# Optimization experiments

Hardware: AMD Instinct MI355X
Metric: run time of the kernel (lower is better)

The kernel has to match this reference:

```python
import jax, jax.numpy as jnp
import numpy as np

N_HEAD = 12
NEG_INF = -1e30


def setup_inputs() -> dict:
    key = jax.random.key(0)
    ks = jax.random.split(key, 12)
    bs, q_len, c_len, d = 2, 2048, 2048, 768
    s = 1.0 / np.sqrt(d)
    return {
        "query": jax.random.normal(ks[0], (bs, q_len, d), jnp.float32),
        "context": jax.random.normal(ks[1], (bs, c_len, d), jnp.float32),
        "c_mask": jax.random.randint(ks[2], (bs, c_len), 0, 2, jnp.int32),
        "Wq_w": jax.random.normal(ks[3], (d, d), jnp.float32) * s,
        "Wq_b": jnp.zeros((d,), jnp.float32),
        "Wk_w": jax.random.normal(ks[4], (d, d), jnp.float32) * s,
        "Wk_b": jnp.zeros((d,), jnp.float32),
        "Wv_w": jax.random.normal(ks[5], (d, d), jnp.float32) * s,
        "Wv_b": jnp.zeros((d,), jnp.float32),
        "fc_w": jax.random.normal(ks[6], (d, d), jnp.float32) * s,
        "fc_b": jnp.zeros((d,), jnp.float32),
    }


def reference(query, context, c_mask, Wq_w, Wq_b, Wk_w, Wk_b, Wv_w, Wv_b, fc_w, fc_b):
    bs, q_len, d = query.shape
    c_len = context.shape[1]
    d_k = d // N_HEAD
    a = 1.0 / np.sqrt(d_k)

    # QKV projections (torch Linear: y = x @ W.T + b), split into heads
    q = (query @ Wq_w.T + Wq_b).reshape(bs, q_len, N_HEAD, d_k)
    k = (context @ Wk_w.T + Wk_b).reshape(bs, c_len, N_HEAD, d_k)
    v = (context @ Wv_w.T + Wv_b).reshape(bs, c_len, N_HEAD, d_k)

    # scores [bs, n_head, q_len, c_len]
    s = jnp.einsum('bqhd,bchd->bhqc', q, k) * a

    # mask_logits: s * m + (1 - m) * -1e30, mask broadcast over heads and q
    m = c_mask.astype(s.dtype)[:, None, None, :]
    s = s * m + (1.0 - m) * NEG_INF

    p = jax.nn.softmax(s, axis=-1)  # dropout p=0.0 -> identity

    out = jnp.einsum('bhqc,bchd->bqhd', p, v).reshape(bs, q_len, d)
    return out @ fc_w.T + fc_b
```

## Files before the change

### kernel.cpp

```cpp
#include <hip/hip_runtime.h>
#include <cstdint>

#define D_MODEL 768
#define NH      12
#define DKH     64
#define SEQ     2048
#define BS      2
#define MROWS   (BS*SEQ)

typedef __bf16 bf16x8 __attribute__((ext_vector_type(8)));
typedef float  f32x4  __attribute__((ext_vector_type(4)));
typedef unsigned int u32_as1 __attribute__((address_space(1)));
typedef unsigned int u32_as3 __attribute__((address_space(3)));

__device__ __forceinline__ void gld16(const void* g, void* l) {
  __builtin_amdgcn_global_load_lds((const u32_as1*)g, (u32_as3*)l, 16, 0, 0);
}
__device__ __forceinline__ unsigned short f2bf(float x) {
  return __builtin_bit_cast(unsigned short, (__bf16)x);
}

__global__ void cvt2(const float* __restrict__ a, const float* __restrict__ b,
                     unsigned short* __restrict__ oa, unsigned short* __restrict__ ob) {
  const float* in = blockIdx.y ? b : a;
  unsigned short* out = blockIdx.y ? ob : oa;
  int i = blockIdx.x * 256 + threadIdx.x;
  float4 v = reinterpret_cast<const float4*>(in)[i];
  ushort4 o; o.x = f2bf(v.x); o.y = f2bf(v.y); o.z = f2bf(v.z); o.w = f2bf(v.w);
  reinterpret_cast<ushort4*>(out)[i] = o;
}
__global__ void cvt4(const float* __restrict__ a, const float* __restrict__ b,
                     const float* __restrict__ c, const float* __restrict__ d,
                     unsigned short* __restrict__ oa, unsigned short* __restrict__ ob,
                     unsigned short* __restrict__ oc, unsigned short* __restrict__ od) {
  const float* in; unsigned short* out;
  switch (blockIdx.y) {
    case 0: in = a; out = oa; break;
    case 1: in = b; out = ob; break;
    case 2: in = c; out = oc; break;
    default: in = d; out = od; break;
  }
  int i = blockIdx.x * 256 + threadIdx.x;
  float4 v = reinterpret_cast<const float4*>(in)[i];
  ushort4 o; o.x = f2bf(v.x); o.y = f2bf(v.y); o.z = f2bf(v.z); o.w = f2bf(v.w);
  reinterpret_cast<ushort4*>(out)[i] = o;
}

__global__ void mask_bf(const int* __restrict__ m, unsigned short* __restrict__ o) {
  int i = blockIdx.x * 256 + threadIdx.x;
  o[i] = f2bf(m[i] ? 1.0f : 0.0f);
}

template<bool OUT_F32>
__device__ __forceinline__ void gemm64x128_body(
    const unsigned short* __restrict__ A, const unsigned short* __restrict__ B,
    const float* __restrict__ bias, int biasRow, void* __restrict__ Cout,
    int ldc, int m0, int n0, float outScale, const int* __restrict__ colMask)
{
  __shared__ alignas(16) char sA[2][8192];
  __shared__ alignas(16) char sB[2][16384];
  const int tid = threadIdx.x;
  const int w = tid >> 6, l = tid & 63;
  const int g16 = l >> 4, c16 = l & 15;
  const int wr = (w >> 1) * 32, wc = (w & 1) * 64;

  auto stageA = [&](int kt, char* dst) {
#pragma unroll
    for (int i = 0; i < 2; i++) {
      int ch = w * 2 + i;
      int X = ch * 1024 + l * 16;
      int row = X >> 7;
      int sl = ((X >> 4) & 7) ^ (row & 7);
      gld16(A + (size_t)(m0 + row) * 768 + kt + sl * 8, dst + ch * 1024);
    }
  };
  auto stageB = [&](int kt, char* dst) {
#pragma unroll
    for (int i = 0; i < 4; i++) {
      int ch = w * 4 + i;
      int X = ch * 1024 + l * 16;
      int row = X >> 7;
      int sl = ((X >> 4) & 7) ^ (row & 7);
      gld16(B + (size_t)(n0 + row) * 768 + kt + sl * 8, dst + ch * 1024);
    }
  };

  f32x4 acc[2][4];
#pragma unroll
  for (int m = 0; m < 2; m++)
#pragma unroll
    for (int n = 0; n < 4; n++) acc[m][n] = f32x4{0.f, 0.f, 0.f, 0.f};

  stageA(0, sA[0]);
  stageB(0, sB[0]);
  __syncthreads();
  int cur = 0;
  for (int kt = 0; kt < 768; kt += 64) {
    if (kt + 64 < 768) {
      stageA(kt + 64, sA[cur ^ 1]);
      stageB(kt + 64, sB[cur ^ 1]);
    }
    __builtin_amdgcn_s_setprio(1);
#pragma unroll
    for (int kk = 0; kk < 2; kk++) {
      bf16x8 af[2], bq[4];
#pragma unroll
      for (int m = 0; m < 2; m++) {
        int row = wr + m * 16 + c16, slot = kk * 4 + g16;
        af[m] = *(const bf16x8*)(sA[cur] + row * 128 + ((slot ^ (row & 7)) << 4));
      }
#pragma unroll
      for (int n = 0; n < 4; n++) {
        int row = wc + n * 16 + c16, slot = kk * 4 + g16;
        bq[n] = *(const bf16x8*)(sB[cur] + row * 128 + ((slot ^ (row & 7)) << 4));
      }
#pragma unroll
      for (int m = 0; m < 2; m++)
#pragma unroll
        for (int n = 0; n < 4; n++)
          acc[m][n] = __builtin_amdgcn_mfma_f32_16x16x32_bf16(af[m], bq[n], acc[m][n], 0, 0, 0);
    }
    __builtin_amdgcn_s_setprio(0);
    __syncthreads();
    cur ^= 1;
  }

#pragma unroll
  for (int m = 0; m < 2; m++)
#pragma unroll
    for (int n = 0; n < 4; n++)
#pragma unroll
      for (int r = 0; r < 4; r++) {
        int row = m0 + wr + m * 16 + g16 * 4 + r;
        int col = n0 + wc + n * 16 + c16;
        float v = (acc[m][n][r] + (biasRow ? bias[row] : bias[col])) * outScale;
        if (colMask) v *= (float)colMask[col];
        if constexpr (OUT_F32) ((float*)Cout)[(size_t)row * ldc + col] = v;
        else ((unsigned short*)Cout)[(size_t)row * ldc + col] = f2bf(v);
      }
}

#define QSCALE 0.1803368801111f

__global__ __launch_bounds__(256, 2) void gemm_qkv(
    const unsigned short* __restrict__ q_bf, const unsigned short* __restrict__ c_bf,
    const unsigned short* __restrict__ wq, const unsigned short* __restrict__ wk,
    const unsigned short* __restrict__ wv,
    const float* __restrict__ bq, const float* __restrict__ bk,
    const float* __restrict__ bv, const int* __restrict__ cmask,
    unsigned short* __restrict__ Qb, unsigned short* __restrict__ Kb,
    unsigned short* __restrict__ Vtb)
{
  const int x = blockIdx.x;
  const int lin = (x & 7) * 48 + (x >> 3);
  if (blockIdx.y == 0) {
    gemm64x128_body<false>(q_bf, wq, bq, 0, Qb, 768, (lin / 6) * 64, (lin % 6) * 128,
                           QSCALE, nullptr);
  } else if (blockIdx.y == 1) {
    gemm64x128_body<false>(c_bf, wk, bk, 0, Kb, 768, (lin / 6) * 64, (lin % 6) * 128,
                           1.0f, nullptr);
  } else {
    gemm64x128_body<false>(wv, c_bf, bv, 1, Vtb, 4096, (lin % 12) * 64, (lin / 12) * 128,
                           1.0f, cmask);
  }
}

__global__ __launch_bounds__(256, 2) void gemm_fc(
    const unsigned short* __restrict__ Ob, const unsigned short* __restrict__ wf,
    const float* __restrict__ fb, float* __restrict__ out)
{
  const int x = blockIdx.x;
  const int lin = (x & 7) * 48 + (x >> 3);
  gemm64x128_body<true>(Ob, wf, fb, 0, out, 768, (lin / 6) * 64, (lin % 6) * 128,
                        1.0f, nullptr);
}

__global__ __launch_bounds__(256, 4) void attn_kernel(
    const unsigned short* __restrict__ Qb, const unsigned short* __restrict__ Kb,
    const unsigned short* __restrict__ Vt, const unsigned short* __restrict__ maskbf,
    unsigned short* __restrict__ Ob)
{
  __shared__ alignas(16) char sK[2][8192];
  __shared__ alignas(16) char sV[2][8192];
  __shared__ alignas(16) char sP[8192];
  const int tid = threadIdx.x, w = tid >> 6, l = tid & 63;
  const int g16 = l >> 4, c16 = l & 15;
  const int flat = blockIdx.x;
  const int xcd = flat & 7, sidx = flat >> 3;
  const int p = xcd + 8 * (sidx >> 5);
  const int qt = sidx & 31;
  const int h = p % 12, b = p / 12;
  const int qrow0 = b * SEQ + qt * 64;
  const int crow0 = b * SEQ;

  bf16x8 qa[2];
  {
    const unsigned short* qp =
        Qb + (size_t)(qrow0 + w * 16 + c16) * D_MODEL + h * DKH + g16 * 8;
    qa[0] = *(const bf16x8*)(qp);
    qa[1] = *(const bf16x8*)(qp + 32);
  }

  auto stageK = [&](int ct, int buf) {
#pragma unroll
    for (int i = 0; i < 2; i++) {
      int ch = w * 2 + i;
      int X = ch * 1024 + l * 16;
      int row = X >> 7;
      int sl = ((X >> 4) & 7) ^ (row & 7);
      gld16(Kb + (size_t)(crow0 + ct + row) * D_MODEL + h * DKH + sl * 8,
            sK[buf] + ch * 1024);
    }
  };
  auto stageV = [&](int ct, int buf) {
#pragma unroll
    for (int i = 0; i < 2; i++) {
      int ch = w * 2 + i;
      int X = ch * 1024 + l * 16;
      int row = X >> 7;
      int sl = ((X >> 4) & 7) ^ (row & 7);
      gld16(Vt + (size_t)(h * DKH + row) * (size_t)MROWS + crow0 + ct + sl * 8,
            sV[buf] + ch * 1024);
    }
  };

  f32x4 accO[4], accL;
#pragma unroll
  for (int n = 0; n < 4; n++) accO[n] = f32x4{0.f, 0.f, 0.f, 0.f};
  accL = f32x4{0.f, 0.f, 0.f, 0.f};

  stageK(0, 0); stageV(0, 0);
  __syncthreads();
  int cur = 0;

  for (int ct = 0; ct < SEQ; ct += 64) {
    if (ct + 64 < SEQ) { stageK(ct + 64, cur ^ 1); stageV(ct + 64, cur ^ 1); }

    bf16x8 mfrag[2];
#pragma unroll
    for (int kk = 0; kk < 2; kk++)
      mfrag[kk] = *(const bf16x8*)(maskbf + crow0 + ct + kk * 32 + g16 * 8);

    f32x4 s[4];
#pragma unroll
    for (int n = 0; n < 4; n++) s[n] = f32x4{0.f, 0.f, 0.f, 0.f};
    __builtin_amdgcn_s_setprio(1);
#pragma unroll
    for (int kk = 0; kk < 2; kk++) {
      bf16x8 kf[4];
#pragma unroll
      for (int n = 0; n < 4; n++) {
        int row = n * 16 + c16, slot = kk * 4 + g16;
        kf[n] = *(const bf16x8*)(sK[cur] + row * 128 + ((slot ^ (row & 7)) << 4));
      }
#pragma unroll
      for (int n = 0; n < 4; n++)
        s[n] = __builtin_amdgcn_mfma_f32_16x16x32_bf16(qa[kk], kf[n], s[n], 0, 0, 0);
    }
    __builtin_amdgcn_s_setprio(0);

#pragma unroll
    for (int r = 0; r < 4; r++) {
      int prow = g16 * 4 + r;
#pragma unroll
      for (int n = 0; n < 4; n++) {
        float pv = __builtin_amdgcn_exp2f(s[n][r]);
        int slot = n * 2 + (c16 >> 3);
        int addr = w * 2048 + prow * 128 + ((slot ^ (prow & 7)) << 4) + (c16 & 7) * 2;
        *(__bf16*)(sP + addr) = (__bf16)pv;
      }
    }

    __builtin_amdgcn_s_setprio(1);
#pragma unroll
    for (int kk = 0; kk < 2; kk++) {
      bf16x8 pa, vf[4];
      {
        int prow = c16, slot = kk * 4 + g16;
        pa = *(const bf16x8*)(sP + w * 2048 + prow * 128 + ((slot ^ (prow & 7)) << 4));
      }
#pragma unroll
      for (int n = 0; n < 4; n++) {
        int vrow = n * 16 + c16, slot = kk * 4 + g16;
        vf[n] = *(const bf16x8*)(sV[cur] + vrow * 128 + ((slot ^ (vrow & 7)) << 4));
      }
#pragma unroll
      for (int n = 0; n < 4; n++)
        accO[n] = __builtin_amdgcn_mfma_f32_16x16x32_bf16(pa, vf[n], accO[n], 0, 0, 0);
      accL = __builtin_amdgcn_mfma_f32_16x16x32_bf16(pa, mfrag[kk], accL, 0, 0, 0);
    }
    __builtin_amdgcn_s_setprio(0);

    __syncthreads();
    cur ^= 1;
  }

#pragma unroll
  for (int r = 0; r < 4; r++) {
    float inv = 1.0f / accL[r];
#pragma unroll
    for (int n = 0; n < 4; n++) {
      int row = qrow0 + w * 16 + g16 * 4 + r;
      int col = h * DKH + n * 16 + c16;
      Ob[(size_t)row * D_MODEL + col] = f2bf(accO[n][r] * inv);
    }
  }
}

extern "C" void kernel_launch(void* const* d_in, const int* in_sizes, int n_in,
                              void* d_out, int out_size, void* d_ws, size_t ws_size,
                              hipStream_t stream) {
  const float* query   = (const float*)d_in[0];
  const float* context = (const float*)d_in[1];
  const int*   cmask   = (const int*)d_in[2];
  const float* Wq_w = (const float*)d_in[3];
  const float* Wq_b = (const float*)d_in[4];
  const float* Wk_w = (const float*)d_in[5];
  const float* Wk_b = (const float*)d_in[6];
  const float* Wv_w = (const float*)d_in[7];
  const float* Wv_b = (const float*)d_in[8];
  const float* fc_w = (const float*)d_in[9];
  const float* fc_b = (const float*)d_in[10];
  float* out = (float*)d_out;

  unsigned short* ws   = (unsigned short*)d_ws;
  const size_t NQ = (size_t)MROWS * D_MODEL;
  const size_t NW = (size_t)D_MODEL * D_MODEL;
  unsigned short* q_bf = ws;
  unsigned short* c_bf = q_bf + NQ;
  unsigned short* Qb   = c_bf + NQ;
  unsigned short* Kb   = Qb + NQ;
  unsigned short* Vtb  = Kb + NQ;
  unsigned short* Ob   = Vtb + NQ;
  unsigned short* wq   = Ob + NQ;
  unsigned short* wk   = wq + NW;
  unsigned short* wv   = wk + NW;
  unsigned short* wf   = wv + NW;
  unsigned short* maskbf = q_bf;

  cvt2<<<dim3(NQ / 4 / 256, 2), 256, 0, stream>>>(query, context, q_bf, c_bf);
  cvt4<<<dim3(NW / 4 / 256, 4), 256, 0, stream>>>(Wq_w, Wk_w, Wv_w, fc_w, wq, wk, wv, wf);

  gemm_qkv<<<dim3(384, 3), 256, 0, stream>>>(
      q_bf, c_bf, wq, wk, wv, Wq_b, Wk_b, Wv_b, cmask, Qb, Kb, Vtb);

  mask_bf<<<MROWS / 256, 256, 0, stream>>>(cmask, maskbf);

  attn_kernel<<<768, 256, 0, stream>>>(Qb, Kb, Vtb, maskbf, Ob);

  gemm_fc<<<384, 256, 0, stream>>>(Ob, wf, fc_b, out);
}
```

Measured before the change: 100.3 us.

## Double attention query tile to 128 rows per block for K/V reuse

Each attention block now processes 128 query rows instead of 64, with every wave handling two 16-row sub-tiles that share the K and V fragments loaded from shared memory. This halves the number of blocks and the total K/V staging traffic from global memory per unit of work, and amortizes LDS reads of K/V across two MFMA rows. In exchange, register and LDS use per block roughly doubles, launch bounds drop to 2 blocks per SIMD group, and only 384 blocks are launched, which may underfill the 256 CUs and reduce latency hiding.

```diff
diff --git a/kernel.cpp b/kernel.cpp
--- a/kernel.cpp
+++ b/kernel.cpp
@@ -175,30 +175,31 @@
                         1.0f, nullptr);
 }
 
-__global__ __launch_bounds__(256, 4) void attn_kernel(
+__global__ __launch_bounds__(256, 2) void attn_kernel(
     const unsigned short* __restrict__ Qb, const unsigned short* __restrict__ Kb,
     const unsigned short* __restrict__ Vt, const unsigned short* __restrict__ maskbf,
     unsigned short* __restrict__ Ob)
 {
   __shared__ alignas(16) char sK[2][8192];
   __shared__ alignas(16) char sV[2][8192];
-  __shared__ alignas(16) char sP[8192];
+  __shared__ alignas(16) char sP[16384];
   const int tid = threadIdx.x, w = tid >> 6, l = tid & 63;
   const int g16 = l >> 4, c16 = l & 15;
   const int flat = blockIdx.x;
   const int xcd = flat & 7, sidx = flat >> 3;
-  const int p = xcd + 8 * (sidx >> 5);
-  const int qt = sidx & 31;
+  const int p = xcd + 8 * (sidx >> 4);
+  const int qt = sidx & 15;
   const int h = p % 12, b = p / 12;
-  const int qrow0 = b * SEQ + qt * 64;
+  const int qrow0 = b * SEQ + qt * 128;
   const int crow0 = b * SEQ;
 
-  bf16x8 qa[2];
-  {
+  bf16x8 qa[2][2];
+#pragma unroll
+  for (int m = 0; m < 2; m++) {
     const unsigned short* qp =
-        Qb + (size_t)(qrow0 + w * 16 + c16) * D_MODEL + h * DKH + g16 * 8;
-    qa[0] = *(const bf16x8*)(qp);
-    qa[1] = *(const bf16x8*)(qp + 32);
+        Qb + (size_t)(qrow0 + w * 32 + m * 16 + c16) * D_MODEL + h * DKH + g16 * 8;
+    qa[m][0] = *(const bf16x8*)(qp);
+    qa[m][1] = *(const bf16x8*)(qp + 32);
   }
 
   auto stageK = [&](int ct, int buf) {
@@ -224,10 +225,13 @@
     }
   };
 
-  f32x4 accO[4], accL;
-#pragma unroll
-  for (int n = 0; n < 4; n++) accO[n] = f32x4{0.f, 0.f, 0.f, 0.f};
-  accL = f32x4{0.f, 0.f, 0.f, 0.f};
+  f32x4 accO[2][4], accL[2];
+#pragma unroll
+  for (int m = 0; m < 2; m++) {
+#pragma unroll
+    for (int n = 0; n < 4; n++) accO[m][n] = f32x4{0.f, 0.f, 0.f, 0.f};
+    accL[m] = f32x4{0.f, 0.f, 0.f, 0.f};
+  }
 
   stageK(0, 0); stageV(0, 0);
   __syncthreads();
@@ -241,9 +245,11 @@
     for (int kk = 0; kk < 2; kk++)
       mfrag[kk] = *(const bf16x8*)(maskbf + crow0 + ct + kk * 32 + g16 * 8);
 
-    f32x4 s[4];
-#pragma unroll
-    for (int n = 0; n < 4; n++) s[n] = f32x4{0.f, 0.f, 0.f, 0.f};
+    f32x4 s[2][4];
+#pragma unroll
+    for (int m = 0; m < 2; m++)
+#pragma unroll
+      for (int n = 0; n < 4; n++) s[m][n] = f32x4{0.f, 0.f, 0.f, 0.f};
     __builtin_amdgcn_s_setprio(1);
 #pragma unroll
     for (int kk = 0; kk < 2; kk++) {
@@ -254,30 +260,35 @@
         kf[n] = *(const bf16x8*)(sK[cur] + row * 128 + ((slot ^ (row & 7)) << 4));
       }
 #pragma unroll
-      for (int n = 0; n < 4; n++)
-        s[n] = __builtin_amdgcn_mfma_f32_16x16x32_bf16(qa[kk], kf[n], s[n], 0, 0, 0);
+      for (int m = 0; m < 2; m++)
+#pragma unroll
+        for (int n = 0; n < 4; n++)
+          s[m][n] = __builtin_amdgcn_mfma_f32_16x16x32_bf16(qa[m][kk], kf[n], s[m][n], 0, 0, 0);
     }
     __builtin_amdgcn_s_setprio(0);
 
 #pragma unroll
-    for (int r = 0; r < 4; r++) {
-      int prow = g16 * 4 + r;
-#pragma unroll
-      for (int n = 0; n < 4; n++) {
-        float pv = __builtin_amdgcn_exp2f(s[n][r]);
-        int slot = n * 2 + (c16 >> 3);
-        int addr = w * 2048 + prow * 128 + ((slot ^ (prow & 7)) << 4) + (c16 & 7) * 2;
-        *(__bf16*)(sP + addr) = (__bf16)pv;
-      }
-    }
+    for (int m = 0; m < 2; m++)
+#pragma unroll
+      for (int r = 0; r < 4; r++) {
+        int prow = m * 16 + g16 * 4 + r;
+#pragma unroll
+        for (int n = 0; n < 4; n++) {
+          float pv = __builtin_amdgcn_exp2f(s[m][n][r]);
+          int slot = n * 2 + (c16 >> 3);
+          int addr = w * 4096 + prow * 128 + ((slot ^ (prow & 7)) << 4) + (c16 & 7) * 2;
+          *(__bf16*)(sP + addr) = (__bf16)pv;
+        }
+      }
 
     __builtin_amdgcn_s_setprio(1);
 #pragma unroll
     for (int kk = 0; kk < 2; kk++) {
-      bf16x8 pa, vf[4];
-      {
-        int prow = c16, slot = kk * 4 + g16;
-        pa = *(const bf16x8*)(sP + w * 2048 + prow * 128 + ((slot ^ (prow & 7)) << 4));
+      bf16x8 pa[2], vf[4];
+#pragma unroll
+      for (int m = 0; m < 2; m++) {
+        int prow = m * 16 + c16, slot = kk * 4 + g16;
+        pa[m] = *(const bf16x8*)(sP + w * 4096 + prow * 128 + ((slot ^ (prow & 7)) << 4));
       }
 #pragma unroll
       for (int n = 0; n < 4; n++) {
@@ -285,9 +296,12 @@
         vf[n] = *(const bf16x8*)(sV[cur] + vrow * 128 + ((slot ^ (vrow & 7)) << 4));
       }
 #pragma unroll
-      for (int n = 0; n < 4; n++)
-        accO[n] = __builtin_amdgcn_mfma_f32_16x16x32_bf16(pa, vf[n], accO[n], 0, 0, 0);
-      accL = __builtin_amdgcn_mfma_f32_16x16x32_bf16(pa, mfrag[kk], accL, 0, 0, 0);
+      for (int m = 0; m < 2; m++) {
+#pragma unroll
+        for (int n = 0; n < 4; n++)
+          accO[m][n] = __builtin_amdgcn_mfma_f32_16x16x32_bf16(pa[m], vf[n], accO[m][n], 0, 0, 0);
+        accL[m] = __builtin_amdgcn_mfma_f32_16x16x32_bf16(pa[m], mfrag[kk], accL[m], 0, 0, 0);
+      }
     }
     __builtin_amdgcn_s_setprio(0);
 
@@ -296,15 +310,17 @@
   }
 
 #pragma unroll
-  for (int r = 0; r < 4; r++) {
-    float inv = 1.0f / accL[r];
-#pragma unroll
-    for (int n = 0; n < 4; n++) {
-      int row = qrow0 + w * 16 + g16 * 4 + r;
-      int col = h * DKH + n * 16 + c16;
-      Ob[(size_t)row * D_MODEL + col] = f2bf(accO[n][r] * inv);
-    }
-  }
+  for (int m = 0; m < 2; m++)
+#pragma unroll
+    for (int r = 0; r < 4; r++) {
+      float inv = 1.0f / accL[m][r];
+#pragma unroll
+      for (int n = 0; n < 4; n++) {
+        int row = qrow0 + w * 32 + m * 16 + g16 * 4 + r;
+        int col = h * DKH + n * 16 + c16;
+        Ob[(size_t)row * D_MODEL + col] = f2bf(accO[m][n][r] * inv);
+      }
+    }
 }
 
 extern "C" void kernel_launch(void* const* d_in, const int* in_sizes, int n_in,
@@ -346,7 +362,7 @@
 
   mask_bf<<<MROWS / 256, 256, 0, stream>>>(cmask, maskbf);
 
-  attn_kernel<<<768, 256, 0, stream>>>(Qb, Kb, Vtb, maskbf, Ob);
+  attn_kernel<<<384, 256, 0, stream>>>(Qb, Kb, Vtb, maskbf, Ob);
 
   gemm_fc<<<384, 256, 0, stream>>>(Ob, wf, fc_b, out);
 }
```

Measured after the change: 105.1 us. 4.8% more time.
